# Kernel optimization log

Measured on AMD Instinct MI355X. Metric: run time of the kernel, lower is better.

The kernel has to match this reference:

```python
import jax, jax.numpy as jnp
import numpy as np

NUM_HEADS = 16
HEAD_DIM = 64  # d_out // num_heads


def setup_inputs() -> dict:
    key = jax.random.key(0)
    ks = jax.random.split(key, 6)
    d_in, d_out, b, t = 1024, 1024, 2, 2048
    s = 0.02
    return {
        "x": jax.random.normal(ks[0], (b, t, d_in), jnp.float32),
        "Wq": jax.random.normal(ks[1], (d_in, d_out), jnp.float32) * s,
        "Wk": jax.random.normal(ks[2], (d_in, d_out), jnp.float32) * s,
        "Wv": jax.random.normal(ks[3], (d_in, d_out), jnp.float32) * s,
        "Wo": jax.random.normal(ks[4], (d_out, d_out), jnp.float32) * s,
        "bo": jnp.zeros((d_out,), jnp.float32),
    }


def reference(x, Wq, Wk, Wv, Wo, bo):
    b, t, _ = x.shape
    H, hd = NUM_HEADS, HEAD_DIM
    # qkv projections (no bias), split into heads: [b, H, t, hd]
    q = (x @ Wq).reshape(b, t, H, hd).transpose(0, 2, 1, 3)
    k = (x @ Wk).reshape(b, t, H, hd).transpose(0, 2, 1, 3)
    v = (x @ Wv).reshape(b, t, H, hd).transpose(0, 2, 1, 3)
    # raw scores, causal mask (masked_fill with -1e9 BEFORE the 1/sqrt(hd) scale,
    # matching the source exactly), then scaled softmax
    scores = jnp.einsum("bhqd,bhkd->bhqk", q, k)
    causal = jnp.triu(jnp.ones((t, t), dtype=bool), k=1)
    scores = jnp.where(causal[None, None], jnp.float32(-1e9), scores)
    attn = jax.nn.softmax(scores / jnp.sqrt(jnp.float32(hd)), axis=-1)
    # dropout is identity in eval mode
    ctx = jnp.einsum("bhqk,bhkd->bhqd", attn, v)  # [b, H, t, hd]
    ctx = ctx.transpose(0, 2, 1, 3).reshape(b, t, H * hd)
    return ctx @ Wo + bo
```

## Files before the change

### kernel.cpp

```cpp
#include <hip/hip_runtime.h>


#define SEQ   2048
#define DMODEL 1024
#define NH    16
#define HD    64
#define MROWS 4096

typedef __attribute__((ext_vector_type(4))) float f32x4;
typedef __attribute__((ext_vector_type(16))) float f32x16;
typedef __attribute__((ext_vector_type(8))) short short8;
typedef __attribute__((ext_vector_type(4))) unsigned int u32x4;

#define MFMA16(a, b, c) __builtin_amdgcn_mfma_f32_16x16x32_bf16((a), (b), (c), 0, 0, 0)
#define MFMA32(a, b, c) __builtin_amdgcn_mfma_f32_32x32x16_bf16((a), (b), (c), 0, 0, 0)

__device__ __forceinline__ unsigned short f2bf(float f) {
  union { float f; unsigned u; } v; v.f = f;
  return (unsigned short)((v.u + 0x7fffu + ((v.u >> 16) & 1u)) >> 16);
}

__device__ __forceinline__ float exp2x(float x) {
#if __has_builtin(__builtin_amdgcn_exp2f)
  return __builtin_amdgcn_exp2f(x);
#else
  float r; asm("v_exp_f32 %0, %1" : "=v"(r) : "v"(x)); return r;
#endif
}

__device__ __forceinline__ unsigned cvt_pk(float lo, float hi) {
  unsigned r;
  asm volatile("v_cvt_pk_bf16_f32 %0, %1, %2" : "=v"(r) : "v"(lo), "v"(hi));
  return r;
}

__device__ __forceinline__ void pls(unsigned& a, unsigned& b) {
  asm("v_permlane32_swap_b32 %0, %1" : "+v"(a), "+v"(b));
}

__device__ __forceinline__ short8 as_short8(u32x4 v) {
  union { u32x4 u; short8 s; } x; x.u = v; return x.s;
}

__device__ __forceinline__ f32x4 zero4() {
  f32x4 z; z[0] = 0.f; z[1] = 0.f; z[2] = 0.f; z[3] = 0.f; return z;
}

__device__ __forceinline__ void async16(const void* g, void* l) {
  __builtin_amdgcn_global_load_lds(
      (const __attribute__((address_space(1))) unsigned int*)g,
      (__attribute__((address_space(3))) unsigned int*)l, 16, 0, 0);
}

__global__ __launch_bounds__(256) void prep(
    const float* __restrict__ x, const float* __restrict__ Wq,
    const float* __restrict__ Wk, const float* __restrict__ Wv,
    const float* __restrict__ Wo, unsigned short* __restrict__ xb,
    unsigned short* __restrict__ Wt, unsigned short* __restrict__ WoT) {
  __shared__ unsigned short tile[64][65];
  const int bx = blockIdx.x;
  if (bx < 2048) {
    int i = bx * 256 + threadIdx.x;
    const float4* p = (const float4*)x;
    float4 a = p[2 * i];
    float4 b = p[2 * i + 1];
    short8 o;
    o[0] = (short)f2bf(a.x); o[1] = (short)f2bf(a.y);
    o[2] = (short)f2bf(a.z); o[3] = (short)f2bf(a.w);
    o[4] = (short)f2bf(b.x); o[5] = (short)f2bf(b.y);
    o[6] = (short)f2bf(b.z); o[7] = (short)f2bf(b.w);
    *(short8*)&xb[(size_t)i * 8] = o;
    return;
  }
  const int id2 = bx - 2048;
  const int m = id2 >> 8;
  const float* W = (m == 0) ? Wq : (m == 1) ? Wk : (m == 2) ? Wv : Wo;
  unsigned short* D = (m == 3) ? WoT : Wt + (size_t)m * 1024 * 1024;
  const int tid = id2 & 255;
  const int kb = (tid >> 4) * 64, nb = (tid & 15) * 64;
  const int t = threadIdx.x;
  const int tx = t & 63, ty = t >> 6;
#pragma unroll
  for (int rr = 0; rr < 16; rr++) {
    int r = ty * 16 + rr;
    tile[r][tx] = f2bf(W[(size_t)(kb + r) * 1024 + nb + tx]);
  }
  __syncthreads();
#pragma unroll
  for (int rr = 0; rr < 16; rr++) {
    int r = ty * 16 + rr;
    D[(size_t)(nb + r) * 1024 + kb + tx] = tile[tx][r];
  }
}

template <int MODE, int WMF>
__global__ __launch_bounds__(256) void gemm_bt(
    const unsigned short* __restrict__ A, const unsigned short* __restrict__ Bt,
    unsigned short* __restrict__ Qo, unsigned short* __restrict__ Ko,
    unsigned short* __restrict__ Vo, float* __restrict__ out,
    const float* __restrict__ bo) {
  constexpr int K = 1024;
  constexpr int BM = WMF * 32;
  constexpr int NT = K / 32;
  __shared__ __align__(16) unsigned short smem[3 * BM * 32 + 3 * 128 * 32];
  unsigned short* Asb = smem;
  unsigned short* Bsb = smem + 3 * BM * 32;
  const int t = threadIdx.x;
  const int lane = t & 63;
  const int w = t >> 6;
  const int lr = lane & 15, kf = lane >> 4;
  const int wr = w >> 1, wc = w & 1;

  const int nwg = gridDim.x * gridDim.y;
  const int id = blockIdx.y * gridDim.x + blockIdx.x;
  const int swz = (id & 7) * (nwg >> 3) + (id >> 3);
  const int bx = swz % gridDim.x, by = swz / gridDim.x;

  const int rowbase = bx * BM;
  const int colbase = by * 128;

  const unsigned short* Ab = A + (size_t)rowbase * K;
  const unsigned short* Bb = Bt + (size_t)colbase * K;

  f32x4 acc[WMF][4];
#pragma unroll
  for (int m = 0; m < WMF; m++)
#pragma unroll
    for (int n = 0; n < 4; n++) acc[m][n] = zero4();

  auto stage = [&](int buf, int kt) {
    int k0 = kt * 32;
#pragma unroll
    for (int i = 0; i < BM / 64; i++) {
      int f = i * 256 + t;
      int c = f ^ ((f >> 3) & 3);
      int row = c >> 2;
      int col = (c & 3) << 3;
      async16(Ab + (size_t)row * K + k0 + col,
              (char*)(Asb + (size_t)buf * BM * 32) + (size_t)f * 16);
    }
#pragma unroll
    for (int i = 0; i < 2; i++) {
      int f = i * 256 + t;
      int c = f ^ ((f >> 3) & 3);
      int row = c >> 2;
      int col = (c & 3) << 3;
      async16(Bb + (size_t)row * K + k0 + col,
              (char*)(Bsb + (size_t)buf * 128 * 32) + (size_t)f * 16);
    }
  };

  stage(0, 0);
  stage(1, 1);

  for (int kt = 0; kt < NT; kt++) {
    if (kt + 2 < NT) {
      stage((kt + 2) % 3, kt + 2);
      if constexpr (MODE == 0) asm volatile("s_waitcnt vmcnt(8)" ::: "memory");
      else                     asm volatile("s_waitcnt vmcnt(6)" ::: "memory");
    } else if (kt + 1 < NT) {
      if constexpr (MODE == 0) asm volatile("s_waitcnt vmcnt(4)" ::: "memory");
      else                     asm volatile("s_waitcnt vmcnt(3)" ::: "memory");
    } else {
      asm volatile("s_waitcnt vmcnt(0)" ::: "memory");
    }
    __builtin_amdgcn_s_barrier();

    const unsigned short* As = Asb + (size_t)(kt % 3) * BM * 32;
    const unsigned short* Bs = Bsb + (size_t)(kt % 3) * 128 * 32;
    short8 av[WMF], bv[4];
#pragma unroll
    for (int m = 0; m < WMF; m++) {
      int row = wr * (WMF * 16) + m * 16 + lr;
      int idx = (row * 32 + kf * 8) ^ (((row >> 1) & 3) << 3);
      av[m] = *(const short8*)&As[idx];
    }
#pragma unroll
    for (int n = 0; n < 4; n++) {
      int row = wc * 64 + n * 16 + lr;
      int idx = (row * 32 + kf * 8) ^ (((row >> 1) & 3) << 3);
      bv[n] = *(const short8*)&Bs[idx];
    }
    __builtin_amdgcn_s_setprio(1);
#pragma unroll
    for (int m = 0; m < WMF; m++)
#pragma unroll
      for (int n = 0; n < 4; n++) acc[m][n] = MFMA16(av[m], bv[n], acc[m][n]);
    __builtin_amdgcn_s_setprio(0);
    __builtin_amdgcn_s_barrier();
  }

  if constexpr (MODE == 0) {
    if (colbase < 2048) {
      const int selq = colbase >> 10;
      unsigned short* dst = selq ? Ko : Qo;
      const float sc = selq ? 1.0f : 0.18033688011112042f;
#pragma unroll
      for (int n = 0; n < 4; n++) {
        int c = colbase + wc * 64 + n * 16 + lr;
        int hh = (c >> 6) & 15;
        int dd = c & 63;
#pragma unroll
        for (int m = 0; m < WMF; m++) {
          int r0 = rowbase + wr * (WMF * 16) + m * 16 + kf * 4;
#pragma unroll
          for (int i = 0; i < 4; i++) {
            int r = r0 + i;
            int bi = r >> 11;
            int tq = r & 2047;
            dst[((size_t)(bi * NH + hh) * SEQ + tq) * HD + dd] = f2bf(acc[m][n][i] * sc);
          }
        }
      }
    } else {
      unsigned short* tr = smem;
#pragma unroll
      for (int n = 0; n < 4; n++) {
        int ccol = wc * 64 + n * 16 + lr;
#pragma unroll
        for (int m = 0; m < WMF; m++) {
#pragma unroll
          for (int i = 0; i < 4; i++) {
            int rrow = wr * (WMF * 16) + m * 16 + kf * 4 + i;
            tr[ccol * 136 + rrow] = f2bf(acc[m][n][i]);
          }
        }
      }
      __syncthreads();
      const int bi2 = rowbase >> 11;
      const int tq0 = rowbase & 2047;
#pragma unroll
      for (int k2 = 0; k2 < 8; k2++) {
        int u = k2 * 256 + t;
        int cc = u >> 4, seg = u & 15;
        int c = colbase + cc;
        int hh = (c >> 6) & 15, dd = c & 63;
        short8 v8 = *(const short8*)&tr[cc * 136 + seg * 8];
        *(short8*)&Vo[((size_t)(bi2 * NH + hh) * HD + dd) * SEQ + tq0 + seg * 8] = v8;
      }
    }
  } else {
#pragma unroll
    for (int n = 0; n < 4; n++) {
      int c = colbase + wc * 64 + n * 16 + lr;
      float bias = bo[c];
#pragma unroll
      for (int m = 0; m < WMF; m++) {
        int r0 = rowbase + wr * (WMF * 16) + m * 16 + kf * 4;
#pragma unroll
        for (int i = 0; i < 4; i++) {
          out[(size_t)(r0 + i) * 1024 + c] = acc[m][n][i] + bias;
        }
      }
    }
  }
}

__global__ __launch_bounds__(256) void attn_fwd(
    const unsigned short* __restrict__ Q, const unsigned short* __restrict__ K,
    const unsigned short* __restrict__ Vt, unsigned short* __restrict__ ctx) {
  const int bh = blockIdx.x;
  const int y = blockIdx.y;
  const int qt = (y < 8) ? (15 - y) : (y - 8);
  const int bi = bh >> 4, hh = bh & 15;
  const int t = threadIdx.x, lane = t & 63, w = t >> 6;
  const int qc = lane & 31, hi = lane >> 5;

  __shared__ __align__(16) unsigned short Ks[2][2][64 * 64];
  __shared__ __align__(16) unsigned short Vs[2][2][64 * 64];

  const unsigned short* Qb = Q + (size_t)bh * SEQ * HD;
  const unsigned short* Kb = K + (size_t)bh * SEQ * HD;
  const unsigned short* Vb = Vt + (size_t)bh * HD * SEQ;

  const int qrow = qt * 128 + w * 32;
  short8 qv[4];
#pragma unroll
  for (int c = 0; c < 4; c++)
    qv[c] = *(const short8*)&Qb[(size_t)(qrow + qc) * HD + c * 16 + hi * 8];

  f32x16 o0, o1;
#pragma unroll
  for (int i = 0; i < 16; i++) { o0[i] = 0.f; o1[i] = 0.f; }
  float l_acc = 0.f;

  const int ktmax = 2 * qt + (w >> 1);
  const int NP = qt + 1;

  auto stage = [&](int buf, int p) {
#pragma unroll
    for (int sub = 0; sub < 2; sub++) {
      int kt = 2 * p + sub;
#pragma unroll
      for (int i2 = 0; i2 < 2; i2++) {
        int f = i2 * 256 + t;
        int c = f ^ ((f >> 3) & 7);
        async16(Kb + (size_t)kt * 64 * HD + (size_t)c * 8,
                (char*)&Ks[buf][sub][0] + (size_t)f * 16);
        int d = c >> 3, ko = (c & 7) << 3;
        async16(Vb + (size_t)d * SEQ + (size_t)kt * 64 + ko,
                (char*)&Vs[buf][sub][0] + (size_t)f * 16);
      }
    }
  };

  auto tile = [&](const unsigned short* Kt, const unsigned short* Vtile, int kt) {
    f32x16 s0, s1;
#pragma unroll
    for (int i = 0; i < 16; i++) { s0[i] = 0.f; s1[i] = 0.f; }
    __builtin_amdgcn_s_setprio(1);
#pragma unroll
    for (int c = 0; c < 4; c++) {
      int i0 = (qc * 64 + c * 16 + hi * 8) ^ ((qc & 7) << 3);
      s0 = MFMA32(*(const short8*)&Kt[i0], qv[c], s0);
      int r1 = 32 + qc;
      int i1 = (r1 * 64 + c * 16 + hi * 8) ^ ((r1 & 7) << 3);
      s1 = MFMA32(*(const short8*)&Kt[i1], qv[c], s1);
    }
    __builtin_amdgcn_s_setprio(0);

    if (kt == ktmax) {
      const int qg = qrow + qc;
#pragma unroll
      for (int reg = 0; reg < 16; reg++) {
        int rloc = (reg & 3) + 8 * (reg >> 2) + 4 * hi;
        int kg = kt * 64 + rloc;
        if (kg > qg) s0[reg] = -1e30f;
        if (kg + 32 > qg) s1[reg] = -1e30f;
      }
    }

    unsigned w0[8], w1[8];
    float psA = 0.f, psB = 0.f;
#pragma unroll
    for (int j = 0; j < 8; j++) {
      float a0 = exp2x(s0[2 * j]), b0 = exp2x(s0[2 * j + 1]);
      float a1 = exp2x(s1[2 * j]), b1 = exp2x(s1[2 * j + 1]);
      psA += a0 + b0;
      psB += a1 + b1;
      w0[j] = cvt_pk(a0, b0);
      w1[j] = cvt_pk(a1, b1);
    }
    l_acc += psA + psB;

    __builtin_amdgcn_s_setprio(1);
#pragma unroll
    for (int h2 = 0; h2 < 2; h2++) {
      unsigned* pw = h2 ? w1 : w0;
#pragma unroll
      for (int cc = 0; cc < 2; cc++) {
        unsigned a0 = pw[cc * 4 + 0], b0 = pw[cc * 4 + 2];
        unsigned a1 = pw[cc * 4 + 1], b1 = pw[cc * 4 + 3];
        pls(a0, b0);
        pls(a1, b1);
        u32x4 pf; pf[0] = a0; pf[1] = a1; pf[2] = b0; pf[3] = b1;
        short8 pfrag = as_short8(pf);
        int c2 = h2 * 2 + cc;
        int ia = (qc * 64 + c2 * 16 + hi * 8) ^ ((qc & 7) << 3);
        o0 = MFMA32(*(const short8*)&Vtile[ia], pfrag, o0);
        int rb = 32 + qc;
        int ib = (rb * 64 + c2 * 16 + hi * 8) ^ ((rb & 7) << 3);
        o1 = MFMA32(*(const short8*)&Vtile[ib], pfrag, o1);
      }
    }
    __builtin_amdgcn_s_setprio(0);
  };

  stage(0, 0);
  int cur = 0;

  for (int p = 0; p < NP; p++) {
    if (p + 1 < NP) {
      stage(cur ^ 1, p + 1);
      asm volatile("s_waitcnt vmcnt(8)" ::: "memory");
    } else {
      asm volatile("s_waitcnt vmcnt(0)" ::: "memory");
    }
    __builtin_amdgcn_s_barrier();

    if (2 * p <= ktmax)     tile(&Ks[cur][0][0], &Vs[cur][0][0], 2 * p);
    if (2 * p + 1 <= ktmax) tile(&Ks[cur][1][0], &Vs[cur][1][0], 2 * p + 1);

    __builtin_amdgcn_s_barrier();
    cur ^= 1;
  }

  float l = l_acc + __shfl_xor(l_acc, 32);
  float inv = 1.0f / l;
  const size_t rowoff = ((size_t)bi * SEQ + qrow + qc) * DMODEL + hh * HD;
#pragma unroll
  for (int g = 0; g < 4; g++) {
    unsigned pa = cvt_pk(o0[4 * g] * inv, o0[4 * g + 1] * inv);
    unsigned pb = cvt_pk(o0[4 * g + 2] * inv, o0[4 * g + 3] * inv);
    uint2 vv; vv.x = pa; vv.y = pb;
    *(uint2*)&ctx[rowoff + 8 * g + 4 * hi] = vv;
    unsigned pc = cvt_pk(o1[4 * g] * inv, o1[4 * g + 1] * inv);
    unsigned pd = cvt_pk(o1[4 * g + 2] * inv, o1[4 * g + 3] * inv);
    uint2 ww; ww.x = pc; ww.y = pd;
    *(uint2*)&ctx[rowoff + 32 + 8 * g + 4 * hi] = ww;
  }
}

extern "C" void kernel_launch(void* const* d_in, const int* in_sizes, int n_in,
                              void* d_out, int out_size, void* d_ws, size_t ws_size,
                              hipStream_t stream) {
  const float* x  = (const float*)d_in[0];
  const float* Wq = (const float*)d_in[1];
  const float* Wk = (const float*)d_in[2];
  const float* Wv = (const float*)d_in[3];
  const float* Wo = (const float*)d_in[4];
  const float* bo = (const float*)d_in[5];
  float* out = (float*)d_out;

  unsigned short* xb   = (unsigned short*)d_ws;
  unsigned short* Wt   = xb + (size_t)MROWS * DMODEL;
  unsigned short* WoT  = Wt + (size_t)3 * 1024 * 1024;
  unsigned short* Qb   = WoT + (size_t)1024 * 1024;
  unsigned short* Kb   = Qb + (size_t)MROWS * DMODEL;
  unsigned short* Vb   = Kb + (size_t)MROWS * DMODEL;
  unsigned short* ctxb = Vb + (size_t)MROWS * DMODEL;

  prep<<<3072, 256, 0, stream>>>(x, Wq, Wk, Wv, Wo, xb, Wt, WoT);

  gemm_bt<0, 4><<<dim3(32, 24), 256, 0, stream>>>(xb, Wt, Qb, Kb, Vb, nullptr, nullptr);
  attn_fwd<<<dim3(32, 16), 256, 0, stream>>>(Qb, Kb, Vb, ctxb);
  gemm_bt<1, 2><<<dim3(64, 8), 256, 0, stream>>>(ctxb, WoT, nullptr, nullptr, nullptr, out, bo);
}
```

Baseline: 106.2 us.

## Double-buffer GEMM with 64-wide K stages to halve barriers

```diff
diff --git a/kernel.cpp b/kernel.cpp
--- a/kernel.cpp
+++ b/kernel.cpp
@@ -101,10 +101,12 @@
     const float* __restrict__ bo) {
   constexpr int K = 1024;
   constexpr int BM = WMF * 32;
-  constexpr int NT = K / 32;
-  __shared__ __align__(16) unsigned short smem[3 * BM * 32 + 3 * 128 * 32];
+  constexpr int NW = K / 64;
+  constexpr int ASZ = BM * 32;
+  constexpr int BSZ = 128 * 32;
+  __shared__ __align__(16) unsigned short smem[4 * ASZ + 4 * BSZ];
   unsigned short* Asb = smem;
-  unsigned short* Bsb = smem + 3 * BM * 32;
+  unsigned short* Bsb = smem + 4 * ASZ;
   const int t = threadIdx.x;
   const int lane = t & 63;
   const int w = t >> 6;
@@ -128,46 +130,34 @@
 #pragma unroll
     for (int n = 0; n < 4; n++) acc[m][n] = zero4();
 
-  auto stage = [&](int buf, int kt) {
-    int k0 = kt * 32;
-#pragma unroll
-    for (int i = 0; i < BM / 64; i++) {
-      int f = i * 256 + t;
-      int c = f ^ ((f >> 3) & 3);
-      int row = c >> 2;
-      int col = (c & 3) << 3;
-      async16(Ab + (size_t)row * K + k0 + col,
-              (char*)(Asb + (size_t)buf * BM * 32) + (size_t)f * 16);
-    }
-#pragma unroll
-    for (int i = 0; i < 2; i++) {
-      int f = i * 256 + t;
-      int c = f ^ ((f >> 3) & 3);
-      int row = c >> 2;
-      int col = (c & 3) << 3;
-      async16(Bb + (size_t)row * K + k0 + col,
-              (char*)(Bsb + (size_t)buf * 128 * 32) + (size_t)f * 16);
+  auto stage = [&](int buf, int wi) {
+#pragma unroll
+    for (int sub = 0; sub < 2; sub++) {
+      int k0 = (2 * wi + sub) * 32;
+      unsigned short* Ad = Asb + ((size_t)buf * 2 + sub) * ASZ;
+      unsigned short* Bd = Bsb + ((size_t)buf * 2 + sub) * BSZ;
+#pragma unroll
+      for (int i = 0; i < BM / 64; i++) {
+        int f = i * 256 + t;
+        int c = f ^ ((f >> 3) & 3);
+        int row = c >> 2;
+        int col = (c & 3) << 3;
+        async16(Ab + (size_t)row * K + k0 + col, (char*)Ad + (size_t)f * 16);
+      }
+#pragma unroll
+      for (int i = 0; i < 2; i++) {
+        int f = i * 256 + t;
+        int c = f ^ ((f >> 3) & 3);
+        int row = c >> 2;
+        int col = (c & 3) << 3;
+        async16(Bb + (size_t)row * K + k0 + col, (char*)Bd + (size_t)f * 16);
+      }
     }
   };
 
-  stage(0, 0);
-  stage(1, 1);
-
-  for (int kt = 0; kt < NT; kt++) {
-    if (kt + 2 < NT) {
-      stage((kt + 2) % 3, kt + 2);
-      if constexpr (MODE == 0) asm volatile("s_waitcnt vmcnt(8)" ::: "memory");
-      else                     asm volatile("s_waitcnt vmcnt(6)" ::: "memory");
-    } else if (kt + 1 < NT) {
-      if constexpr (MODE == 0) asm volatile("s_waitcnt vmcnt(4)" ::: "memory");
-      else                     asm volatile("s_waitcnt vmcnt(3)" ::: "memory");
-    } else {
-      asm volatile("s_waitcnt vmcnt(0)" ::: "memory");
-    }
-    __builtin_amdgcn_s_barrier();
-
-    const unsigned short* As = Asb + (size_t)(kt % 3) * BM * 32;
-    const unsigned short* Bs = Bsb + (size_t)(kt % 3) * 128 * 32;
+  auto compute = [&](int buf, int sub) {
+    const unsigned short* As = Asb + ((size_t)buf * 2 + sub) * ASZ;
+    const unsigned short* Bs = Bsb + ((size_t)buf * 2 + sub) * BSZ;
     short8 av[WMF], bv[4];
 #pragma unroll
     for (int m = 0; m < WMF; m++) {
@@ -187,7 +177,26 @@
 #pragma unroll
       for (int n = 0; n < 4; n++) acc[m][n] = MFMA16(av[m], bv[n], acc[m][n]);
     __builtin_amdgcn_s_setprio(0);
+  };
+
+  stage(0, 0);
+  int cur = 0;
+
+  for (int wi = 0; wi < NW; wi++) {
+    if (wi + 1 < NW) {
+      stage(cur ^ 1, wi + 1);
+      if constexpr (MODE == 0) asm volatile("s_waitcnt vmcnt(8)" ::: "memory");
+      else                     asm volatile("s_waitcnt vmcnt(6)" ::: "memory");
+    } else {
+      asm volatile("s_waitcnt vmcnt(0)" ::: "memory");
+    }
     __builtin_amdgcn_s_barrier();
+
+    compute(cur, 0);
+    compute(cur, 1);
+
+    __builtin_amdgcn_s_barrier();
+    cur ^= 1;
   }
 
   if constexpr (MODE == 0) {
```

Result: no change. 104.8 us (-1.3%).
